# Kernel tuning notes

Hardware: AMD Instinct MI355X
Metric: run time of the kernel (lower is better)

Reference implementation:

```python
import jax, jax.numpy as jnp
import numpy as np

HEADS = 8
DIM_HEAD = 64


def setup_inputs() -> dict:
    key = jax.random.key(0)
    ks = jax.random.split(key, 5)
    B, N, C, coor = 2, 2048, 256, 3
    dim_inner = HEADS * DIM_HEAD  # 512
    # weight scale 1/16 ~ 1/sqrt(256) keeps softmax logits in a sane range
    w_scale = 1.0 / 16.0
    return {
        "x": jax.random.normal(ks[0], (B, N, C, coor), dtype=jnp.float32),
        "Wq": jax.random.normal(ks[1], (dim_inner, C), dtype=jnp.float32) * w_scale,
        "Wk": jax.random.normal(ks[2], (dim_inner, C), dtype=jnp.float32) * w_scale,
        "Wv": jax.random.normal(ks[3], (dim_inner, C), dtype=jnp.float32) * w_scale,
        "Wo": jax.random.normal(ks[4], (C, dim_inner), dtype=jnp.float32) * w_scale,
    }


def _split_heads(t, B, N, coor):
    # b n (h d) c -> b h n (d c)
    t = t.reshape(B, N, HEADS, DIM_HEAD, coor)
    t = t.transpose(0, 2, 1, 3, 4)
    return t.reshape(B, HEADS, N, DIM_HEAD * coor)


def reference(x, Wq, Wk, Wv, Wo):
    B, N, C, coor = x.shape
    # VNLinear: einsum('... i c, o i -> ... o c')
    q = jnp.einsum('bnic,oi->bnoc', x, Wq)
    k = jnp.einsum('bnic,oi->bnoc', x, Wk)
    v = jnp.einsum('bnic,oi->bnoc', x, Wv)
    q = _split_heads(q, B, N, coor)  # (B, H, N, d*c)
    k = _split_heads(k, B, N, coor)
    v = _split_heads(v, B, N, coor)
    scale = (DIM_HEAD * coor) ** -0.5
    sim = jnp.einsum('bhie,bhje->bhij', q, k) * scale  # (B, H, N, N)
    attn = jax.nn.softmax(sim, axis=-1)
    out = jnp.einsum('bhij,bhje->bhie', attn, v)  # (B, H, N, d*c)
    # b h n (d c) -> b n (h d) c
    out = out.reshape(B, HEADS, N, DIM_HEAD, coor).transpose(0, 2, 1, 3, 4)
    out = out.reshape(B, N, HEADS * DIM_HEAD, coor)
    # to_out VNLinear
    return jnp.einsum('bnic,oi->bnoc', out, Wo)  # (B, N, C, 3)
```

## Files before the change

### kernel.cpp

```cpp
#include <hip/hip_runtime.h>

#define HEADS 8
#define DH 64
#define CO 3
#define E 192
#define NSEQ 2048
#define BATCH 2
#define CIN 256
#define DINNER 512
#define NTOK 4096
#define BHTOT 16

typedef __attribute__((ext_vector_type(8))) short bf16x8;
typedef __attribute__((ext_vector_type(4))) short bf16x4;
typedef __attribute__((ext_vector_type(4))) float f32x4;
typedef __attribute__((ext_vector_type(4))) float float4v;

static __device__ inline short f2bf(float f) {
  union { float f; unsigned u; } v; v.f = f;
  unsigned r = (v.u + 0x7FFFu + ((v.u >> 16) & 1u)) >> 16;
  return (short)r;
}

static __device__ inline float bf2f(short s) {
  union { unsigned u; float f; } a;
  a.u = ((unsigned)(unsigned short)s) << 16;
  return a.f;
}

static __device__ inline void load_lds16(const short* g, short* l) {
  __builtin_amdgcn_global_load_lds(
      (const __attribute__((address_space(1))) void*)g,
      (__attribute__((address_space(3))) void*)l, 16, 0, 0);
}


__global__ __launch_bounds__(256) void prep(const float* __restrict__ x,
                                            const float* __restrict__ Wq,
                                            const float* __restrict__ Wk,
                                            const float* __restrict__ Wv,
                                            const float* __restrict__ Wo,
                                            short* __restrict__ xcp,
                                            short* __restrict__ wqkvp,
                                            short* __restrict__ wop) {
  int tid = threadIdx.x;
  if (blockIdx.x < 256) {
    __shared__ short st[12288];
    int mt = blockIdx.x;
    const float* xb = x + (size_t)mt * 12288;
#pragma unroll
    for (int r = 0; r < 12; r++) {
      int idx4 = r * 256 + tid;
      float4v v = *(const float4v*)(xb + idx4 * 4);
#pragma unroll
      for (int e = 0; e < 4; e++) {
        int fp = idx4 * 4 + e;
        int ti = fp / 3, c = fp - ti * 3;
        int tl = ti >> 8, i = ti & 255;
        int ks = i >> 5, qd = (i >> 3) & 3, j = i & 7;
        st[c * 4096 + ks * 512 + (qd * 16 + tl) * 8 + j] = f2bf(v[e]);
      }
    }
    __syncthreads();
    short* dst = xcp;
#pragma unroll
    for (int rep = 0; rep < 6; rep++) {
      int g = rep * 256 + tid;
      int c = g >> 9, rem = g & 511;
      *(bf16x8*)(dst + ((size_t)(c * 256 + mt) * 8) * 512 + rem * 8) =
          *(const bf16x8*)&st[c * 4096 + rem * 8];
    }
    return;
  }
  int idx = (blockIdx.x - 256) * 256 + tid;
  const float qscale = 0.07216878364870323f * 1.4426950408889634f;
  if (idx < 1536 * 256) {
    int o = idx >> 8, i = idx & 255;
    float v;
    if (o < 512) v = Wq[idx] * qscale;
    else if (o < 1024) v = Wk[idx - 512 * 256];
    else v = Wv[idx - 1024 * 256];
    int nt = o >> 4, ln = o & 15, ks = i >> 5, qd = (i >> 3) & 3, j = i & 7;
    wqkvp[((size_t)(nt * 8 + ks)) * 512 + (qd * 16 + ln) * 8 + j] = f2bf(v);
  } else {
    int j0 = idx - 1536 * 256;
    if (j0 < 256 * 512) {
      int o2 = j0 >> 9, i = j0 & 511;
      int nt = o2 >> 4, ln = o2 & 15, ks = i >> 5, qd = (i >> 3) & 3, j = i & 7;
      wop[((size_t)(nt * 16 + ks)) * 512 + (qd * 16 + ln) * 8 + j] = f2bf(Wo[j0]);
    }
  }
}

__global__ __launch_bounds__(256, 4) void qkv_gemm(const short* __restrict__ xcp,
                                                   const short* __restrict__ wqkvp,
                                                   short* __restrict__ qp,
                                                   short* __restrict__ kp,
                                                   short* __restrict__ vp) {
  __shared__ __align__(16) short pool[17408];
  int c = blockIdx.z, ntb = blockIdx.x, mtb = blockIdx.y;
  int tid = threadIdx.x, wave = tid >> 6, lane = tid & 63;
  int ln = lane & 15, quad = lane >> 4;
  int wm = wave >> 1, wn = wave & 1;

  const short* gA = xcp + ((size_t)(c * 256 + mtb * 8) * 8) * 512;
  const short* gB = wqkvp + ((size_t)(ntb * 8) * 8) * 512;

  f32x4 acc[4][4] = {};
#pragma unroll
  for (int i = 0; i < 2; i++) {
    int q = tid + 256 * i, mf = q >> 6, l = q & 63;
    load_lds16(gA + (size_t)(mf * 8) * 512 + l * 8, pool + q * 8);
  }
  for (int ks = 0; ks < 8; ks++) {
    int b = ks & 1;
    __syncthreads();
    if (ks < 7) {
#pragma unroll
      for (int i = 0; i < 2; i++) {
        int q = tid + 256 * i, mf = q >> 6, l = q & 63;
        load_lds16(gA + (size_t)(mf * 8 + ks + 1) * 512 + l * 8,
                   pool + (b ^ 1) * 4096 + q * 8);
      }
    }
    const short* As = pool + b * 4096;
    bf16x8 af[4], bfr[4];
#pragma unroll
    for (int j = 0; j < 4; j++)
      bfr[j] = *(const bf16x8*)(gB + (size_t)((wn * 4 + j) * 8 + ks) * 512 + lane * 8);
#pragma unroll
    for (int i = 0; i < 4; i++) af[i] = *(const bf16x8*)&As[(wm * 4 + i) * 512 + lane * 8];
#pragma unroll
    for (int i = 0; i < 4; i++)
#pragma unroll
      for (int j = 0; j < 4; j++)
        acc[i][j] = __builtin_amdgcn_mfma_f32_16x16x32_bf16(af[i], bfr[j], acc[i][j], 0, 0, 0);
  }

  int mat = ntb >> 2;
  int b0 = mtb >> 4;
  if (mat < 2) {
    __syncthreads();
    short* tp = pool;
#pragma unroll
    for (int i = 0; i < 4; i++)
#pragma unroll
      for (int j = 0; j < 4; j++)
#pragma unroll
        for (int jj = 0; jj < 4; jj++)
          tp[(wm * 64 + i * 16 + quad * 4 + jj) * 136 + wn * 64 + j * 16 + ln] =
              f2bf(acc[i][j][jj]);
    __syncthreads();
    short* dst = (mat == 0) ? qp : kp;
    int h0 = (ntb & 3) * 2;
#pragma unroll
    for (int rep = 0; rep < 8; rep++) {
      int gi = rep * 256 + tid;
      int l2 = gi & 15, qd = (gi >> 4) & 3, nf2 = (gi >> 6) & 3,
          esp = (gi >> 8) & 1, hh = (gi >> 9) & 1, kt2 = gi >> 10;
      int tl = kt2 * 64 + nf2 * 16 + l2;
      bf16x8 val = *(const bf16x8*)&tp[tl * 136 + hh * 64 + (esp * 4 + qd) * 8];
      int bhx = b0 * 8 + h0 + hh;
      int kt = (mtb * 2 + kt2) & 31;
      int es = c * 2 + esp;
      size_t off = (((size_t)((bhx * 32 + kt) * 24) + es * 4 + nf2) * 64 +
                    (size_t)(qd * 16 + l2)) * 8;
      *(bf16x8*)(dst + off) = val;
    }
  } else {
#pragma unroll
    for (int i = 0; i < 4; i++) {
      int kt = (mtb * 2 + wm) & 31;
      int ks2 = (i >> 1) & 1;
      int qd2 = (i * 2 + (quad >> 1)) & 3;
#pragma unroll
      for (int j = 0; j < 4; j++) {
        int o = ntb * 128 + wn * 64 + j * 16 + ln;
        int oo = o & 511, h = oo >> 6, d = oo & 63;
        int ef = c * 4 + (d >> 4), l2v = d & 15;
        int bhx = b0 * 8 + h;
        size_t off = ((size_t)((bhx * 32 + kt) * 24 + ks2 * 12 + ef)) * 512 +
                     (qd2 * 16 + l2v) * 8 + (quad & 1) * 4;
        bf16x4 val = { f2bf(acc[i][j][0]), f2bf(acc[i][j][1]),
                       f2bf(acc[i][j][2]), f2bf(acc[i][j][3]) };
        *(bf16x4*)(vp + off) = val;
      }
    }
  }
}

__global__ __launch_bounds__(256, 2) void attn(const short* __restrict__ qp,
                                               const short* __restrict__ kp,
                                               const short* __restrict__ vp,
                                               short* __restrict__ opart,
                                               float* __restrict__ lpart) {
  __shared__ __align__(16) short pool[29696];
  int pair = blockIdx.x, qt = blockIdx.y;
  int bh = pair & 15, kh = pair >> 4;
  int tid = threadIdx.x, wave = tid >> 6, lane = tid & 63;
  int ln = lane & 15, quad = lane >> 4;
  short* Pl = pool + 24576;

  bf16x8 qf[2][6];
#pragma unroll
  for (int rg = 0; rg < 2; rg++) {
    int fi = wave * 2 + rg;
    const short* qb = qp +
        ((size_t)(bh * 32 + qt * 2 + (fi >> 2)) * 24 + (fi & 3)) * 512 + lane * 8;
#pragma unroll
    for (int es = 0; es < 6; es++) qf[rg][es] = *(const bf16x8*)(qb + es * 2048);
  }

  float l_r[2][4] = {};
  f32x4 acc[2][12] = {};
  const short* gKb = kp + (size_t)(bh * 32 + kh * 16) * 12288;
  const short* gVb = vp + (size_t)(bh * 32 + kh * 16) * 12288;

  auto stage = [&](int k32, int buf) {
    const short* g64K = gKb + (size_t)(k32 >> 1) * 12288;
    const short* g64V = gVb + (size_t)(k32 >> 1) * 12288;
    int half = k32 & 1;
    short* Kd = pool + buf * 6144;
    short* Vd = pool + 12288 + buf * 6144;
#pragma unroll
    for (int i = 0; i < 3; i++) {
      int q = i * 256 + tid;
      int f = q >> 6, l = q & 63;
      int es = f >> 1, nfl = f & 1;
      load_lds16(g64K + (size_t)(es * 4 + half * 2 + nfl) * 512 + l * 8, Kd + q * 8);
      load_lds16(g64V + (size_t)(half * 12 + f) * 512 + l * 8, Vd + q * 8);
    }
  };

  stage(0, 0);
  for (int kt = 0; kt < 32; kt++) {
    int b = kt & 1;
    __syncthreads();
    if (kt < 31) stage(kt + 1, b ^ 1);
    const short* Kl = pool + b * 6144;
    const short* Vl = pool + 12288 + b * 6144;

    f32x4 s[2][2] = {};
#pragma unroll
    for (int es = 0; es < 6; es++) {
#pragma unroll
      for (int nfl = 0; nfl < 2; nfl++) {
        bf16x8 kf = *(const bf16x8*)&Kl[(es * 2 + nfl) * 512 + lane * 8];
        s[0][nfl] = __builtin_amdgcn_mfma_f32_16x16x32_bf16(qf[0][es], kf, s[0][nfl], 0, 0, 0);
        s[1][nfl] = __builtin_amdgcn_mfma_f32_16x16x32_bf16(qf[1][es], kf, s[1][nfl], 0, 0, 0);
      }
    }

#pragma unroll
    for (int rg = 0; rg < 2; rg++)
#pragma unroll
      for (int jj = 0; jj < 4; jj++)
#pragma unroll
        for (int nfl = 0; nfl < 2; nfl++) {
          float p = __builtin_amdgcn_exp2f(s[rg][nfl][jj]);
          union { float f; unsigned u; } v; v.f = p;
          Pl[((wave * 2 + rg) * 16 + quad * 4 + jj) * 40 + nfl * 16 + ln] =
              (short)((v.u + 0x8000u) >> 16);
          l_r[rg][jj] += p;
        }

    bf16x8 pa[2];
#pragma unroll
    for (int rg = 0; rg < 2; rg++)
      pa[rg] = *(const bf16x8*)&Pl[((wave * 2 + rg) * 16 + ln) * 40 + quad * 8];

#pragma unroll
    for (int ef = 0; ef < 12; ef++) {
      bf16x8 v0 = *(const bf16x8*)&Vl[ef * 512 + lane * 8];
      acc[0][ef] = __builtin_amdgcn_mfma_f32_16x16x32_bf16(pa[0], v0, acc[0][ef], 0, 0, 0);
      acc[1][ef] = __builtin_amdgcn_mfma_f32_16x16x32_bf16(pa[1], v0, acc[1][ef], 0, 0, 0);
    }
  }

#pragma unroll
  for (int rg = 0; rg < 2; rg++)
#pragma unroll
    for (int jj = 0; jj < 4; jj++)
#pragma unroll
      for (int off = 1; off < 16; off <<= 1)
        l_r[rg][jj] += __shfl_xor(l_r[rg][jj], off, 64);

  __syncthreads();
  short* tp = pool;
#pragma unroll
  for (int rg = 0; rg < 2; rg++)
#pragma unroll
    for (int jj = 0; jj < 4; jj++) {
      int row = (wave * 2 + rg) * 16 + quad * 4 + jj;
#pragma unroll
      for (int ef = 0; ef < 12; ef++)
        tp[row * 200 + ef * 16 + ln] = f2bf(acc[rg][ef][jj]);
    }
  __syncthreads();
  const size_t obase = ((size_t)(kh * 16 + bh) * 2048 + qt * 128) * 192;
#pragma unroll
  for (int rep = 0; rep < 12; rep++) {
    int gi = rep * 256 + tid;
    int row = gi / 24, c8 = gi - row * 24;
    *(bf16x8*)(opart + obase + (size_t)row * 192 + c8 * 8) =
        *(const bf16x8*)&tp[row * 200 + c8 * 8];
  }
  int lb = (kh * 16 + bh) * 2048 + qt * 128;
  if (ln == 0) {
#pragma unroll
    for (int rg = 0; rg < 2; rg++)
#pragma unroll
      for (int jj = 0; jj < 4; jj++)
        lpart[lb + (wave * 2 + rg) * 16 + quad * 4 + jj] = l_r[rg][jj];
  }
}

__global__ __launch_bounds__(256, 4) void out_gemm(const short* __restrict__ opart,
                                                   const float* __restrict__ lpart,
                                                   const short* __restrict__ wop,
                                                   float* __restrict__ out) {
  __shared__ __align__(16) short Al[8192];
  int mtb = blockIdx.x, c = blockIdx.y;
  int tid = threadIdx.x, wave = tid >> 6, lane = tid & 63;
  int ln = lane & 15, quad = lane >> 4;
  const size_t HSTR = (size_t)16 * 2048 * 192;

#pragma unroll
  for (int rep = 0; rep < 4; rep++) {
    int g = rep * 256 + tid;
    int d8 = g & 7, h = (g >> 3) & 7, row16 = g >> 6;
    int t = mtb * 16 + row16, b = t >> 11, n = t & 2047;
    int bh = b * 8 + h;
    size_t src = ((size_t)bh * 2048 + n) * 192 + c * 64 + d8 * 8;
    bf16x8 o1 = *(const bf16x8*)(opart + src);
    bf16x8 o2 = *(const bf16x8*)(opart + HSTR + src);
    float l = lpart[bh * 2048 + n] + lpart[32768 + bh * 2048 + n];
    float inv = 1.f / l;
    bf16x8 r;
#pragma unroll
    for (int j = 0; j < 8; j++) r[j] = f2bf((bf2f(o1[j]) + bf2f(o2[j])) * inv);
    int i0 = h * 64 + d8 * 8;
    int ks = i0 >> 5, qd = d8 & 3;
    *(bf16x8*)&Al[ks * 512 + (qd * 16 + row16) * 8] = r;
  }
  __syncthreads();

  f32x4 acc[4] = {};
  for (int ks = 0; ks < 16; ks++) {
    bf16x8 af = *(const bf16x8*)&Al[ks * 512 + lane * 8];
#pragma unroll
    for (int jf = 0; jf < 4; jf++) {
      int nt = wave * 4 + jf;
      bf16x8 bfr = *(const bf16x8*)(wop + (size_t)(nt * 16 + ks) * 512 + lane * 8);
      acc[jf] = __builtin_amdgcn_mfma_f32_16x16x32_bf16(af, bfr, acc[jf], 0, 0, 0);
    }
  }
#pragma unroll
  for (int jf = 0; jf < 4; jf++) {
    int o2 = (wave * 4 + jf) * 16 + ln;
#pragma unroll
    for (int jj = 0; jj < 4; jj++) {
      int t = mtb * 16 + quad * 4 + jj;
      out[((size_t)t * 256 + o2) * 3 + c] = acc[jf][jj];
    }
  }
}

extern "C" void kernel_launch(void* const* d_in, const int* in_sizes, int n_in,
                              void* d_out, int out_size, void* d_ws, size_t ws_size,
                              hipStream_t stream) {
  const float* x  = (const float*)d_in[0];
  const float* Wq = (const float*)d_in[1];
  const float* Wk = (const float*)d_in[2];
  const float* Wv = (const float*)d_in[3];
  const float* Wo = (const float*)d_in[4];
  float* out = (float*)d_out;

  short* ws    = (short*)d_ws;
  short* xcp   = ws;
  short* wqkvp = xcp + 3 * NTOK * CIN;
  short* wop   = wqkvp + 1536 * 256;
  short* qp    = wop + 256 * 512;
  short* kp    = qp + (size_t)BHTOT * NSEQ * E;
  short* vp    = kp + (size_t)BHTOT * NSEQ * E;
  short* opart = vp + (size_t)BHTOT * NSEQ * E;
  float* lpart = (float*)xcp;

  prep<<<2304, 256, 0, stream>>>(x, Wq, Wk, Wv, Wo, xcp, wqkvp, wop);
  qkv_gemm<<<dim3(12, 32, 3), 256, 0, stream>>>(xcp, wqkvp, qp, kp, vp);
  attn<<<dim3(32, 16), 256, 0, stream>>>(qp, kp, vp, opart, lpart);
  out_gemm<<<dim3(256, 3), 256, 0, stream>>>(opart, lpart, wop, out);
}
```

Baseline: 164.4 us.

## Narrow qkv_gemm N-tile and merge coordinates in out_gemm with coalesced stores

qkv_gemm now uses 64-wide output tiles, one head per block, and doubles the grid so more blocks run and the epilogue indexing gets simpler. out_gemm computes all three coordinates in one block, so each Wo fragment load is reused across three MFMAs. Results are staged through LDS so they can be written to the interleaved (t,o,c) output as coalesced float4 stores instead of strided scalar stores. The cost is more LDS and registers per out_gemm block, which lowers occupancy, and smaller qkv tiles that reuse less data.

```diff
diff --git a/kernel.cpp b/kernel.cpp
--- a/kernel.cpp
+++ b/kernel.cpp
@@ -97,16 +97,15 @@
                                                    short* __restrict__ qp,
                                                    short* __restrict__ kp,
                                                    short* __restrict__ vp) {
-  __shared__ __align__(16) short pool[17408];
+  __shared__ __align__(16) short pool[9216];
   int c = blockIdx.z, ntb = blockIdx.x, mtb = blockIdx.y;
   int tid = threadIdx.x, wave = tid >> 6, lane = tid & 63;
   int ln = lane & 15, quad = lane >> 4;
   int wm = wave >> 1, wn = wave & 1;
 
   const short* gA = xcp + ((size_t)(c * 256 + mtb * 8) * 8) * 512;
-  const short* gB = wqkvp + ((size_t)(ntb * 8) * 8) * 512;
-
-  f32x4 acc[4][4] = {};
+
+  f32x4 acc[4][2] = {};
 #pragma unroll
   for (int i = 0; i < 2; i++) {
     int q = tid + 256 * i, mf = q >> 6, l = q & 63;
@@ -124,43 +123,44 @@
       }
     }
     const short* As = pool + b * 4096;
-    bf16x8 af[4], bfr[4];
-#pragma unroll
-    for (int j = 0; j < 4; j++)
-      bfr[j] = *(const bf16x8*)(gB + (size_t)((wn * 4 + j) * 8 + ks) * 512 + lane * 8);
+    bf16x8 af[4], bfr[2];
+#pragma unroll
+    for (int j = 0; j < 2; j++)
+      bfr[j] = *(const bf16x8*)(wqkvp +
+          (size_t)((ntb * 4 + wn * 2 + j) * 8 + ks) * 512 + lane * 8);
 #pragma unroll
     for (int i = 0; i < 4; i++) af[i] = *(const bf16x8*)&As[(wm * 4 + i) * 512 + lane * 8];
 #pragma unroll
     for (int i = 0; i < 4; i++)
 #pragma unroll
-      for (int j = 0; j < 4; j++)
+      for (int j = 0; j < 2; j++)
         acc[i][j] = __builtin_amdgcn_mfma_f32_16x16x32_bf16(af[i], bfr[j], acc[i][j], 0, 0, 0);
   }
 
-  int mat = ntb >> 2;
+  int mat = ntb >> 3;
+  int h = ntb & 7;
   int b0 = mtb >> 4;
+  int bhx = b0 * 8 + h;
   if (mat < 2) {
     __syncthreads();
     short* tp = pool;
 #pragma unroll
     for (int i = 0; i < 4; i++)
 #pragma unroll
-      for (int j = 0; j < 4; j++)
+      for (int j = 0; j < 2; j++)
 #pragma unroll
         for (int jj = 0; jj < 4; jj++)
-          tp[(wm * 64 + i * 16 + quad * 4 + jj) * 136 + wn * 64 + j * 16 + ln] =
+          tp[(wm * 64 + i * 16 + quad * 4 + jj) * 72 + wn * 32 + j * 16 + ln] =
               f2bf(acc[i][j][jj]);
     __syncthreads();
     short* dst = (mat == 0) ? qp : kp;
-    int h0 = (ntb & 3) * 2;
-#pragma unroll
-    for (int rep = 0; rep < 8; rep++) {
+#pragma unroll
+    for (int rep = 0; rep < 4; rep++) {
       int gi = rep * 256 + tid;
       int l2 = gi & 15, qd = (gi >> 4) & 3, nf2 = (gi >> 6) & 3,
-          esp = (gi >> 8) & 1, hh = (gi >> 9) & 1, kt2 = gi >> 10;
+          esp = (gi >> 8) & 1, kt2 = (gi >> 9) & 1;
       int tl = kt2 * 64 + nf2 * 16 + l2;
-      bf16x8 val = *(const bf16x8*)&tp[tl * 136 + hh * 64 + (esp * 4 + qd) * 8];
-      int bhx = b0 * 8 + h0 + hh;
+      bf16x8 val = *(const bf16x8*)&tp[tl * 72 + esp * 32 + qd * 8];
       int kt = (mtb * 2 + kt2) & 31;
       int es = c * 2 + esp;
       size_t off = (((size_t)((bhx * 32 + kt) * 24) + es * 4 + nf2) * 64 +
@@ -174,13 +174,10 @@
       int ks2 = (i >> 1) & 1;
       int qd2 = (i * 2 + (quad >> 1)) & 3;
 #pragma unroll
-      for (int j = 0; j < 4; j++) {
-        int o = ntb * 128 + wn * 64 + j * 16 + ln;
-        int oo = o & 511, h = oo >> 6, d = oo & 63;
-        int ef = c * 4 + (d >> 4), l2v = d & 15;
-        int bhx = b0 * 8 + h;
+      for (int j = 0; j < 2; j++) {
+        int ef = c * 4 + wn * 2 + j;
         size_t off = ((size_t)((bhx * 32 + kt) * 24 + ks2 * 12 + ef)) * 512 +
-                     (qd2 * 16 + l2v) * 8 + (quad & 1) * 4;
+                     (qd2 * 16 + ln) * 8 + (quad & 1) * 4;
         bf16x4 val = { f2bf(acc[i][j][0]), f2bf(acc[i][j][1]),
                        f2bf(acc[i][j][2]), f2bf(acc[i][j][3]) };
         *(bf16x4*)(vp + off) = val;
@@ -315,20 +312,22 @@
   }
 }
 
-__global__ __launch_bounds__(256, 4) void out_gemm(const short* __restrict__ opart,
-                                                   const float* __restrict__ lpart,
-                                                   const short* __restrict__ wop,
-                                                   float* __restrict__ out) {
-  __shared__ __align__(16) short Al[8192];
-  int mtb = blockIdx.x, c = blockIdx.y;
+__global__ __launch_bounds__(256) void out_gemm(const short* __restrict__ opart,
+                                                const float* __restrict__ lpart,
+                                                const short* __restrict__ wop,
+                                                float* __restrict__ out) {
+  __shared__ __align__(16) float pool_f[12352];
+  short* Al = (short*)pool_f;
+  int mtb = blockIdx.x;
   int tid = threadIdx.x, wave = tid >> 6, lane = tid & 63;
   int ln = lane & 15, quad = lane >> 4;
   const size_t HSTR = (size_t)16 * 2048 * 192;
 
 #pragma unroll
-  for (int rep = 0; rep < 4; rep++) {
+  for (int rep = 0; rep < 12; rep++) {
     int g = rep * 256 + tid;
-    int d8 = g & 7, h = (g >> 3) & 7, row16 = g >> 6;
+    int c = g >> 10, inner = g & 1023;
+    int d8 = inner & 7, h = (inner >> 3) & 7, row16 = inner >> 6;
     int t = mtb * 16 + row16, b = t >> 11, n = t & 2047;
     int bh = b * 8 + h;
     size_t src = ((size_t)bh * 2048 + n) * 192 + c * 64 + d8 * 8;
@@ -339,30 +338,43 @@
     bf16x8 r;
 #pragma unroll
     for (int j = 0; j < 8; j++) r[j] = f2bf((bf2f(o1[j]) + bf2f(o2[j])) * inv);
-    int i0 = h * 64 + d8 * 8;
-    int ks = i0 >> 5, qd = d8 & 3;
-    *(bf16x8*)&Al[ks * 512 + (qd * 16 + row16) * 8] = r;
+    int ks = h * 2 + (d8 >> 2), qd = d8 & 3;
+    *(bf16x8*)&Al[c * 8192 + ks * 512 + (qd * 16 + row16) * 8] = r;
   }
   __syncthreads();
 
-  f32x4 acc[4] = {};
+  f32x4 acc[3][4] = {};
   for (int ks = 0; ks < 16; ks++) {
-    bf16x8 af = *(const bf16x8*)&Al[ks * 512 + lane * 8];
+    bf16x8 af[3];
+#pragma unroll
+    for (int c = 0; c < 3; c++) af[c] = *(const bf16x8*)&Al[c * 8192 + ks * 512 + lane * 8];
 #pragma unroll
     for (int jf = 0; jf < 4; jf++) {
       int nt = wave * 4 + jf;
       bf16x8 bfr = *(const bf16x8*)(wop + (size_t)(nt * 16 + ks) * 512 + lane * 8);
-      acc[jf] = __builtin_amdgcn_mfma_f32_16x16x32_bf16(af, bfr, acc[jf], 0, 0, 0);
-    }
-  }
-#pragma unroll
-  for (int jf = 0; jf < 4; jf++) {
-    int o2 = (wave * 4 + jf) * 16 + ln;
-#pragma unroll
-    for (int jj = 0; jj < 4; jj++) {
-      int t = mtb * 16 + quad * 4 + jj;
-      out[((size_t)t * 256 + o2) * 3 + c] = acc[jf][jj];
-    }
+#pragma unroll
+      for (int c = 0; c < 3; c++)
+        acc[c][jf] = __builtin_amdgcn_mfma_f32_16x16x32_bf16(af[c], bfr, acc[c][jf], 0, 0, 0);
+    }
+  }
+  __syncthreads();
+#pragma unroll
+  for (int c = 0; c < 3; c++)
+#pragma unroll
+    for (int jf = 0; jf < 4; jf++) {
+      int o2 = (wave * 4 + jf) * 16 + ln;
+#pragma unroll
+      for (int jj = 0; jj < 4; jj++)
+        pool_f[(quad * 4 + jj) * 772 + o2 * 3 + c] = acc[c][jf][jj];
+    }
+  __syncthreads();
+  float* ob = out + (size_t)mtb * 12288;
+#pragma unroll
+  for (int rep = 0; rep < 12; rep++) {
+    int idx = rep * 256 + tid;
+    int row = idx / 192, col4 = idx - row * 192;
+    *(float4v*)(ob + row * 768 + col4 * 4) =
+        *(const float4v*)(pool_f + row * 772 + col4 * 4);
   }
 }
 
@@ -387,7 +399,7 @@
   float* lpart = (float*)xcp;
 
   prep<<<2304, 256, 0, stream>>>(x, Wq, Wk, Wv, Wo, xcp, wqkvp, wop);
-  qkv_gemm<<<dim3(12, 32, 3), 256, 0, stream>>>(xcp, wqkvp, qp, kp, vp);
+  qkv_gemm<<<dim3(24, 32, 3), 256, 0, stream>>>(xcp, wqkvp, qp, kp, vp);
   attn<<<dim3(32, 16), 256, 0, stream>>>(qp, kp, vp, opart, lpart);
-  out_gemm<<<dim3(256, 3), 256, 0, stream>>>(opart, lpart, wop, out);
-}
+  out_gemm<<<256, 256, 0, stream>>>(opart, lpart, wop, out);
+}
```

After: 159.5 us. -3.0%, faster.
